# Kernel optimization log

Hardware: AMD Instinct MI355X
Metric: run time of the kernel (lower is better)

## Reference

```python
import jax, jax.numpy as jnp
import numpy as np
import math

C = 512
B, T = 8, 2048
STRIDE = 2
LN_EPS = 1e-5
EPS = 1e-8


def _ln(x, g, b):
    mu = jnp.mean(x, axis=-1, keepdims=True)
    var = jnp.mean(jnp.square(x - mu), axis=-1, keepdims=True)
    return (x - mu) * jax.lax.rsqrt(var + LN_EPS) * g + b


def _lin(x, w, b):
    # torch Linear: y = x @ W^T + b, W: [out, in]
    return jnp.einsum('btc,oc->bto', x, w) + b


def setup_inputs() -> dict:
    key = jax.random.key(0)
    ks = iter(jax.random.split(key, 40))
    s = 0.02
    d = {'x': jax.random.normal(next(ks), (B, T, C), jnp.float32)}
    # downsample conv: [C_out, C_in, K]
    d['dw'] = jax.random.normal(next(ks), (C, C, 3), jnp.float32) * s
    d['db'] = jnp.zeros((C,), jnp.float32)
    for br in ('cr', 'd', 'c'):
        for p in ('q', 'k', 'v'):
            d[f'w{p}_{br}'] = jax.random.normal(next(ks), (C, C), jnp.float32) * s
            d[f'b{p}_{br}'] = jnp.zeros((C,), jnp.float32)
        d[f'ln_{br}_g'] = jnp.ones((C,), jnp.float32)
        d[f'ln_{br}_b'] = jnp.zeros((C,), jnp.float32)
    d['temp'] = jnp.asarray(0.1, jnp.float32)
    d['gw'] = jax.random.normal(next(ks), (3, 3 * C), jnp.float32) * s  # conv1d k=1 squeezed
    d['gb'] = jnp.zeros((3,), jnp.float32)
    return d


def _forward(x, dw, db, wq_cr, bq_cr, wk_cr, bk_cr, wv_cr, bv_cr, ln_cr_g, ln_cr_b,
             wq_d, bq_d, wk_d, bk_d, wv_d, bv_d, ln_d_g, ln_d_b,
             wq_c, bq_c, wk_c, bk_c, wv_c, bv_c, ln_c_g, ln_c_b,
             temp, gw, gb):
    scale = 1.0 / math.sqrt(C)
    # downsample: Conv1d(k=3, stride, pad=1) on [B,C,T]
    xc = jnp.transpose(x, (0, 2, 1))
    xd = jax.lax.conv_general_dilated(
        xc, dw, window_strides=(STRIDE,), padding=[(1, 1)],
        dimension_numbers=('NCH', 'OIH', 'NCH')) + db[None, :, None]
    x_down = jnp.transpose(xd, (0, 2, 1))  # [B, T//2, C]

    # cross-resolution branch
    q = _lin(x, wq_cr, bq_cr)
    k = _lin(x_down, wk_cr, bk_cr)
    v = _lin(x_down, wv_cr, bv_cr)
    a = jax.nn.softmax(jnp.einsum('btc,bsc->bts', q, k) * scale, axis=-1)
    out_cross = _ln(jnp.einsum('bts,bsc->btc', a, v), ln_cr_g, ln_cr_b)

    # dot-product branch
    q = _lin(x, wq_d, bq_d)
    k = _lin(x, wk_d, bk_d)
    v = _lin(x, wv_d, bv_d)
    a = jax.nn.softmax(jnp.einsum('btc,bsc->bts', q, k) * scale, axis=-1)
    out_dot = _ln(jnp.einsum('bts,bsc->btc', a, v), ln_d_g, ln_d_b)

    # cosine branch with learnable temperature
    q = _lin(x, wq_c, bq_c)
    k = _lin(x, wk_c, bk_c)
    qn = q / (jnp.linalg.norm(q, axis=2, keepdims=True) + EPS)
    kn = k / (jnp.linalg.norm(k, axis=2, keepdims=True) + EPS)
    t = jnp.maximum(temp, 0.01)
    a = jax.nn.softmax(jnp.einsum('btc,bsc->bts', qn, kn) / t, axis=-1)
    v = _lin(x, wv_c, bv_c)
    out_cos = _ln(jnp.einsum('bts,bsc->btc', a, v), ln_c_g, ln_c_b)

    # learned gating fusion (conv1d k=1 == per-position linear over 3C)
    fused = jnp.concatenate([out_cross, out_dot, out_cos], axis=-1)  # [B,T,3C]
    gate = jax.nn.softmax(jnp.einsum('btc,gc->btg', fused, gw) + gb, axis=-1)  # [B,T,3]
    z = (gate[..., 0:1] * out_cross + gate[..., 1:2] * out_dot + gate[..., 2:3] * out_cos)
    return z


def reference(x, dw, db, wq_cr, bq_cr, wk_cr, bk_cr, wv_cr, bv_cr, ln_cr_g, ln_cr_b,
              wq_d, bq_d, wk_d, bk_d, wv_d, bv_d, ln_d_g, ln_d_b,
              wq_c, bq_c, wk_c, bk_c, wv_c, bv_c, ln_c_g, ln_c_b,
              temp, gw, gb):
    return _forward(x, dw, db, wq_cr, bq_cr, wk_cr, bk_cr, wv_cr, bv_cr, ln_cr_g, ln_cr_b,
                    wq_d, bq_d, wk_d, bk_d, wv_d, bv_d, ln_d_g, ln_d_b,
                    wq_c, bq_c, wk_c, bk_c, wv_c, bv_c, ln_c_g, ln_c_b,
                    temp, gw, gb)
```

## Files before the change

kernel.cpp:

```cpp
#include <hip/hip_runtime.h>


typedef __attribute__((ext_vector_type(8))) __bf16 bf16x8;
typedef __attribute__((ext_vector_type(4))) float f32x4;

#define CDIM 512
#define TFULL 2048

#define GLL16(gp, lp)                                                        \
  __builtin_amdgcn_global_load_lds(                                          \
      (const __attribute__((address_space(1))) unsigned int*)(gp),           \
      (__attribute__((address_space(3))) unsigned int*)(lp), 16, 0, 0)

__device__ __forceinline__ unsigned short f2bf(float f) {
  unsigned u = __float_as_uint(f);
  u = (u + 0x7fffu + ((u >> 16) & 1u)) >> 16;
  return (unsigned short)u;
}
__device__ __forceinline__ float bf2f(unsigned short h) {
  return __uint_as_float(((unsigned)h) << 16);
}

__global__ __launch_bounds__(256)
void k_tobf16(const float* __restrict__ src, unsigned short* __restrict__ dst, long n4) {
  long i = (long)blockIdx.x * 256 + threadIdx.x;
  if (i >= n4) return;
  float4 f = reinterpret_cast<const float4*>(src)[i];
  unsigned short o4[4] = {f2bf(f.x), f2bf(f.y), f2bf(f.z), f2bf(f.w)};
  reinterpret_cast<uint2*>(dst)[i] = *reinterpret_cast<const uint2*>(o4);
}

struct WPtrs { const float* p[9]; };
__global__ __launch_bounds__(256)
void k_tobf16w(WPtrs w, unsigned short* __restrict__ dst) {
  int idx = blockIdx.x * 256 + threadIdx.x;
  if (idx >= 9 * 65536) return;
  int m = idx >> 16, off = idx & 65535;
  float4 f = reinterpret_cast<const float4*>(w.p[m])[off];
  unsigned short o4[4] = {f2bf(f.x), f2bf(f.y), f2bf(f.z), f2bf(f.w)};
  reinterpret_cast<uint2*>(dst + (long)m * 262144)[off] = *reinterpret_cast<const uint2*>(o4);
}

__global__ __launch_bounds__(256)
void k_dwreorder(const float* __restrict__ dw, unsigned short* __restrict__ dwb) {
  int idx = blockIdx.x * 256 + threadIdx.x;
  if (idx >= 512 * 1536) return;
  int o = idx / 1536, rem = idx - o * 1536;
  int k = rem >> 9, i = rem & 511;
  dwb[idx] = f2bf(dw[(o * 512 + i) * 3 + k]);
}

__global__ __launch_bounds__(256)
void k_im2col(const float* __restrict__ x, unsigned short* __restrict__ aim) {
  long idx = (long)blockIdx.x * 256 + threadIdx.x;
  if (idx >= (long)8192 * 1536 / 4) return;
  long e = idx * 4;
  int row = (int)(e / 1536);
  int col = (int)(e - (long)row * 1536);
  int b = row >> 10, t = row & 1023;
  int k = col >> 9, i = col & 511;
  int r = 2 * t - 1 + k;
  float4 f = {0.f, 0.f, 0.f, 0.f};
  if (r >= 0) f = *reinterpret_cast<const float4*>(x + ((long)b * TFULL + r) * CDIM + i);
  unsigned short o4[4] = {f2bf(f.x), f2bf(f.y), f2bf(f.z), f2bf(f.w)};
  *reinterpret_cast<uint2*>(aim + e) = *reinterpret_cast<const uint2*>(o4);
}

__global__ __launch_bounds__(256)
void k_gemm(const unsigned short* __restrict__ A,
            const unsigned short* __restrict__ B,
            void* __restrict__ Cp,
            int K, int lda, int ldb, int ldc,
            long sA, long sB, long sC,
            const float* __restrict__ bias,
            float alpha, const float* __restrict__ tempPtr,
            int mode, int ldct) {
  const int gx = gridDim.x;
  const int nwg = gx * gridDim.y;
  int wg = blockIdx.x + gx * blockIdx.y;
  wg = (wg & 7) * (nwg >> 3) + (wg >> 3);
  const int tm0 = (wg % gx) * 128, tn0 = (wg / gx) * 128;
  const int bz = blockIdx.z;
  const unsigned short* Ag = A + (long)bz * sA;
  const unsigned short* Bg = B + (long)bz * sB;

  __shared__ __align__(16) unsigned short smem[32768];

  const int tid = threadIdx.x;
  const int lane = tid & 63;
  const int wave = tid >> 6;
  const int wm = (wave >> 1) * 64, wn = (wave & 1) * 64;
  const int lrow = lane & 15, kq = lane >> 4;

  f32x4 acc[4][4];
#pragma unroll
  for (int i = 0; i < 4; ++i)
#pragma unroll
    for (int j = 0; j < 4; ++j) acc[i][j] = f32x4{0.f, 0.f, 0.f, 0.f};

  const int sr = tid >> 3;
  const int sj = (tid & 7) ^ (sr & 7);
  const unsigned short* aSrc = Ag + (long)(tm0 + sr) * lda + sj * 8;
  const unsigned short* bSrc = Bg + (long)(tn0 + sr) * ldb + sj * 8;

  const int nt = K >> 6;

#define STAGE(kt_, buf_)                                                     \
  {                                                                          \
    unsigned short* aD = smem + (buf_) * 8192 + wave * 512;                  \
    unsigned short* bD = smem + 16384 + (buf_) * 8192 + wave * 512;          \
    _Pragma("unroll")                                                        \
    for (int rd = 0; rd < 4; ++rd) {                                         \
      GLL16(aSrc + (kt_) + (long)rd * 32 * lda, aD + rd * 2048);             \
      GLL16(bSrc + (kt_) + (long)rd * 32 * ldb, bD + rd * 2048);             \
    }                                                                        \
  }

  STAGE(0, 0);

  const int xr = (lrow & 7) << 3;
  for (int t = 0; t < nt; ++t) {
    __syncthreads();
    if (t + 1 < nt) STAGE((t + 1) << 6, (t + 1) & 1);
    const unsigned short* As_ = smem + (t & 1) * 8192;
    const unsigned short* Bs_ = smem + 16384 + (t & 1) * 8192;
    bf16x8 af[4][2], bfv[4][2];
#pragma unroll
    for (int mi = 0; mi < 4; ++mi)
#pragma unroll
      for (int ks = 0; ks < 2; ++ks)
        af[mi][ks] = *reinterpret_cast<const bf16x8*>(
            &As_[(wm + mi * 16 + lrow) * 64 + ((ks * 32 + kq * 8) ^ xr)]);
#pragma unroll
    for (int ni = 0; ni < 4; ++ni)
#pragma unroll
      for (int ks = 0; ks < 2; ++ks)
        bfv[ni][ks] = *reinterpret_cast<const bf16x8*>(
            &Bs_[(wn + ni * 16 + lrow) * 64 + ((ks * 32 + kq * 8) ^ xr)]);
#pragma unroll
    for (int mi = 0; mi < 4; ++mi)
#pragma unroll
      for (int ni = 0; ni < 4; ++ni) {
        acc[mi][ni] = __builtin_amdgcn_mfma_f32_16x16x32_bf16(af[mi][0], bfv[ni][0], acc[mi][ni], 0, 0, 0);
        acc[mi][ni] = __builtin_amdgcn_mfma_f32_16x16x32_bf16(af[mi][1], bfv[ni][1], acc[mi][ni], 0, 0, 0);
      }
  }
#undef STAGE

  if (tempPtr) alpha = 1.0f / fmaxf(*tempPtr, 0.01f);

  if (mode == 1) {
    unsigned short* Cb = (unsigned short*)Cp + (long)bz * sC;
#pragma unroll
    for (int mi = 0; mi < 4; ++mi) {
      int rg = tm0 + wm + mi * 16 + kq * 4;
#pragma unroll
      for (int ni = 0; ni < 4; ++ni) {
        int cg = tn0 + wn + ni * 16 + lrow;
        float bb = bias ? bias[cg] : 0.f;
        f32x4 v = acc[mi][ni];
#pragma unroll
        for (int r = 0; r < 4; ++r)
          Cb[(long)(rg + r) * ldc + cg] = f2bf(v[r] * alpha + bb);
      }
    }
  } else {
    unsigned short* Cb = (unsigned short*)Cp + (long)bz * sC;
#pragma unroll
    for (int mi = 0; mi < 4; ++mi) {
      int rg = tm0 + wm + mi * 16 + kq * 4;
#pragma unroll
      for (int ni = 0; ni < 4; ++ni) {
        int cg = tn0 + wn + ni * 16 + lrow;
        float bb = bias ? bias[cg] : 0.f;
        f32x4 v = acc[mi][ni];
#pragma unroll
        for (int r = 0; r < 4; ++r)
          Cb[(long)cg * ldct + (rg + r)] = f2bf(v[r] * alpha + bb);
      }
    }
  }
}

__global__ __launch_bounds__(512)
void k_gemm256(const unsigned short* __restrict__ A,
               const unsigned short* __restrict__ B,
               unsigned short* __restrict__ C,
               int K, int lda, int ldb, int ldc,
               long sA, long sB, long sC,
               float alpha, const float* __restrict__ tempPtr) {
  const int gx = gridDim.x;
  const int nwg = gx * gridDim.y;
  int wg = blockIdx.x + gx * blockIdx.y;
  wg = (wg & 7) * (nwg >> 3) + (wg >> 3);
  const int tm0 = (wg % gx) * 256, tn0 = (wg / gx) * 256;
  const unsigned short* Ag = A + (long)blockIdx.z * sA;
  const unsigned short* Bg = B + (long)blockIdx.z * sB;

  __shared__ __align__(16) unsigned short smem[32768];

  const int tid = threadIdx.x;
  const int lane = tid & 63;
  const int wave = tid >> 6;
  const int wm = (wave >> 2) * 128, wn = (wave & 3) * 64;
  const int lrow = lane & 15, kq = lane >> 4;

  f32x4 acc[8][4];
#pragma unroll
  for (int i = 0; i < 8; ++i)
#pragma unroll
    for (int j = 0; j < 4; ++j) acc[i][j] = f32x4{0.f, 0.f, 0.f, 0.f};

  const int srow = lane >> 2;
  const int sslot = (lane & 3) ^ ((lane >> 3) & 3);
  const unsigned short* aS0 = Ag + (long)(tm0 + wave * 16 + srow) * lda + sslot * 8;
  const unsigned short* aS1 = aS0 + 128L * lda;
  const unsigned short* bS0 = Bg + (long)(tn0 + wave * 16 + srow) * ldb + sslot * 8;
  const unsigned short* bS1 = bS0 + 128L * ldb;

  const int nt = K >> 5;

#define STAGE256(kt_, buf_)                                                  \
  {                                                                          \
    unsigned short* aD = smem + (buf_) * 8192 + wave * 512;                  \
    unsigned short* bD = smem + 16384 + (buf_) * 8192 + wave * 512;          \
    GLL16(aS0 + (kt_), aD);                                                  \
    GLL16(aS1 + (kt_), aD + 4096);                                           \
    GLL16(bS0 + (kt_), bD);                                                  \
    GLL16(bS1 + (kt_), bD + 4096);                                           \
  }

  STAGE256(0, 0);

  const int xr = ((lrow >> 1) & 3) << 3;
  for (int t = 0; t < nt; ++t) {
    if (t + 1 < nt) {
      STAGE256((t + 1) << 5, (t + 1) & 1);
      asm volatile("s_waitcnt vmcnt(4)" ::: "memory");
    } else {
      asm volatile("s_waitcnt vmcnt(0)" ::: "memory");
    }
    __builtin_amdgcn_s_barrier();
    __builtin_amdgcn_sched_barrier(0);
    const unsigned short* As_ = smem + (t & 1) * 8192;
    const unsigned short* Bs_ = smem + 16384 + (t & 1) * 8192;
    bf16x8 bfv[4];
#pragma unroll
    for (int ni = 0; ni < 4; ++ni)
      bfv[ni] = *reinterpret_cast<const bf16x8*>(
          &Bs_[(wn + ni * 16 + lrow) * 32 + ((kq * 8) ^ xr)]);
#pragma unroll
    for (int mi = 0; mi < 8; ++mi) {
      bf16x8 af = *reinterpret_cast<const bf16x8*>(
          &As_[(wm + mi * 16 + lrow) * 32 + ((kq * 8) ^ xr)]);
#pragma unroll
      for (int ni = 0; ni < 4; ++ni)
        acc[mi][ni] = __builtin_amdgcn_mfma_f32_16x16x32_bf16(af, bfv[ni], acc[mi][ni], 0, 0, 0);
    }
    __builtin_amdgcn_sched_barrier(0);
    if (t + 1 < nt) __builtin_amdgcn_s_barrier();
  }
#undef STAGE256

  if (tempPtr) alpha = 1.0f / fmaxf(*tempPtr, 0.01f);

  C += (long)blockIdx.z * sC;
#pragma unroll
  for (int mi = 0; mi < 8; ++mi) {
    int rg = tm0 + wm + mi * 16 + kq * 4;
#pragma unroll
    for (int ni = 0; ni < 4; ++ni) {
      int cg = tn0 + wn + ni * 16 + lrow;
      f32x4 v = acc[mi][ni];
#pragma unroll
      for (int r = 0; r < 4; ++r)
        C[(long)(rg + r) * ldc + cg] = f2bf(v[r] * alpha);
    }
  }
}

__global__ __launch_bounds__(256)
void k_softmax(unsigned short* __restrict__ S, int cols) {
  const long base = (long)blockIdx.x * cols;
  const int tid = threadIdx.x, lane = tid & 63, wave = tid >> 6;
  const int nv = cols >> 3;
  float f[8];
  float mx = -3.0e38f;
  if (tid < nv) {
    uint4 v = *reinterpret_cast<const uint4*>(S + base + tid * 8);
    const unsigned short* pv = (const unsigned short*)&v;
#pragma unroll
    for (int j = 0; j < 8; ++j) { f[j] = bf2f(pv[j]); mx = fmaxf(mx, f[j]); }
  }
  __shared__ float rmax[4], rsum[4];
#pragma unroll
  for (int o = 32; o > 0; o >>= 1) mx = fmaxf(mx, __shfl_down(mx, o));
  if (lane == 0) rmax[wave] = mx;
  __syncthreads();
  mx = fmaxf(fmaxf(rmax[0], rmax[1]), fmaxf(rmax[2], rmax[3]));
  float sum = 0.f;
  if (tid < nv) {
#pragma unroll
    for (int j = 0; j < 8; ++j) { f[j] = __expf(f[j] - mx); sum += f[j]; }
  }
#pragma unroll
  for (int o = 32; o > 0; o >>= 1) sum += __shfl_down(sum, o);
  if (lane == 0) rsum[wave] = sum;
  __syncthreads();
  const float inv = 1.0f / (rsum[0] + rsum[1] + rsum[2] + rsum[3]);
  if (tid < nv) {
    unsigned short o8[8];
#pragma unroll
    for (int j = 0; j < 8; ++j) o8[j] = f2bf(f[j] * inv);
    *reinterpret_cast<uint4*>(S + base + tid * 8) = *reinterpret_cast<const uint4*>(o8);
  }
}

__global__ __launch_bounds__(256)
void k_l2norm(unsigned short* __restrict__ Q, int ld) {
  const int lane = threadIdx.x & 63, wave = threadIdx.x >> 6;
  const long row = (long)blockIdx.x * 4 + wave;
  unsigned short* p = Q + row * ld + lane * 8;
  uint4 v = *reinterpret_cast<const uint4*>(p);
  const unsigned short* pv = (const unsigned short*)&v;
  float f[8]; float q = 0.f;
#pragma unroll
  for (int j = 0; j < 8; ++j) { f[j] = bf2f(pv[j]); q += f[j] * f[j]; }
#pragma unroll
  for (int o = 32; o > 0; o >>= 1) q += __shfl_xor(q, o);
  float sc = 1.0f / (sqrtf(q) + 1e-8f);
  unsigned short o8[8];
#pragma unroll
  for (int j = 0; j < 8; ++j) o8[j] = f2bf(f[j] * sc);
  *reinterpret_cast<uint4*>(p) = *reinterpret_cast<const uint4*>(o8);
}

__global__ __launch_bounds__(256)
void k_ln_bf(unsigned short* __restrict__ X, const float* __restrict__ g,
             const float* __restrict__ b) {
  const int lane = threadIdx.x & 63, wave = threadIdx.x >> 6;
  const long row = (long)blockIdx.x * 4 + wave;
  unsigned short* p = X + row * CDIM + lane * 8;
  uint4 v = *reinterpret_cast<const uint4*>(p);
  const unsigned short* pv = (const unsigned short*)&v;
  float f[8];
  float s = 0.f, q = 0.f;
#pragma unroll
  for (int j = 0; j < 8; ++j) { f[j] = bf2f(pv[j]); s += f[j]; q += f[j] * f[j]; }
#pragma unroll
  for (int o = 32; o > 0; o >>= 1) { s += __shfl_xor(s, o); q += __shfl_xor(q, o); }
  float mu = s * (1.f / 512.f);
  float var = q * (1.f / 512.f) - mu * mu;
  float rs = rsqrtf(var + 1e-5f);
  float gg[8], bb[8];
  *reinterpret_cast<float4*>(&gg[0]) = *reinterpret_cast<const float4*>(g + lane * 8);
  *reinterpret_cast<float4*>(&gg[4]) = *reinterpret_cast<const float4*>(g + lane * 8 + 4);
  *reinterpret_cast<float4*>(&bb[0]) = *reinterpret_cast<const float4*>(b + lane * 8);
  *reinterpret_cast<float4*>(&bb[4]) = *reinterpret_cast<const float4*>(b + lane * 8 + 4);
  unsigned short o8[8];
#pragma unroll
  for (int j = 0; j < 8; ++j) o8[j] = f2bf((f[j] - mu) * rs * gg[j] + bb[j]);
  *reinterpret_cast<uint4*>(p) = *reinterpret_cast<const uint4*>(o8);
}

__global__ __launch_bounds__(256)
void k_gate(const unsigned short* __restrict__ o0, const unsigned short* __restrict__ o1,
            const unsigned short* __restrict__ o2, const float* __restrict__ gw,
            const float* __restrict__ gb, float* __restrict__ out) {
  __shared__ float gws[3 * 1536];
  for (int i = threadIdx.x; i < 3 * 1536; i += 256) gws[i] = gw[i];
  __syncthreads();
  const int lane = threadIdx.x & 63, wave = threadIdx.x >> 6;
  const long pos = (long)blockIdx.x * 4 + wave;
  const long off = pos * CDIM + lane * 8;
  float a[8], bq[8], cq[8];
  {
    uint4 va = *reinterpret_cast<const uint4*>(o0 + off);
    uint4 vb = *reinterpret_cast<const uint4*>(o1 + off);
    uint4 vc = *reinterpret_cast<const uint4*>(o2 + off);
    const unsigned short* pa = (const unsigned short*)&va;
    const unsigned short* pb = (const unsigned short*)&vb;
    const unsigned short* pc = (const unsigned short*)&vc;
#pragma unroll
    for (int j = 0; j < 8; ++j) { a[j] = bf2f(pa[j]); bq[j] = bf2f(pb[j]); cq[j] = bf2f(pc[j]); }
  }
  float l0 = 0.f, l1 = 0.f, l2 = 0.f;
  const int ch = lane * 8;
#pragma unroll
  for (int j = 0; j < 8; ++j) {
    l0 += a[j] * gws[ch + j] + bq[j] * gws[512 + ch + j] + cq[j] * gws[1024 + ch + j];
    l1 += a[j] * gws[1536 + ch + j] + bq[j] * gws[2048 + ch + j] + cq[j] * gws[2560 + ch + j];
    l2 += a[j] * gws[3072 + ch + j] + bq[j] * gws[3584 + ch + j] + cq[j] * gws[4096 + ch + j];
  }
#pragma unroll
  for (int o = 32; o > 0; o >>= 1) {
    l0 += __shfl_xor(l0, o); l1 += __shfl_xor(l1, o); l2 += __shfl_xor(l2, o);
  }
  l0 += gb[0]; l1 += gb[1]; l2 += gb[2];
  float m = fmaxf(l0, fmaxf(l1, l2));
  float e0 = __expf(l0 - m), e1 = __expf(l1 - m), e2 = __expf(l2 - m);
  float inv = 1.f / (e0 + e1 + e2);
  float g0 = e0 * inv, g1 = e1 * inv, g2 = e2 * inv;
  float r[8];
#pragma unroll
  for (int j = 0; j < 8; ++j) r[j] = g0 * a[j] + g1 * bq[j] + g2 * cq[j];
  *reinterpret_cast<float4*>(out + off) = *reinterpret_cast<const float4*>(&r[0]);
  *reinterpret_cast<float4*>(out + off + 4) = *reinterpret_cast<const float4*>(&r[4]);
}

extern "C" void kernel_launch(void* const* d_in, const int* in_sizes, int n_in,
                              void* d_out, int out_size, void* d_ws, size_t ws_size,
                              hipStream_t stream) {
  (void)in_sizes; (void)n_in; (void)out_size;
  const float* x = (const float*)d_in[0];
  const float* dw = (const float*)d_in[1];
  const float* db = (const float*)d_in[2];
  WPtrs wp;
  wp.p[0] = (const float*)d_in[3];  wp.p[1] = (const float*)d_in[5];
  wp.p[2] = (const float*)d_in[7];  wp.p[3] = (const float*)d_in[11];
  wp.p[4] = (const float*)d_in[13]; wp.p[5] = (const float*)d_in[15];
  wp.p[6] = (const float*)d_in[19]; wp.p[7] = (const float*)d_in[21];
  wp.p[8] = (const float*)d_in[23];
  const float* bq_cr = (const float*)d_in[4];
  const float* bk_cr = (const float*)d_in[6];
  const float* bv_cr = (const float*)d_in[8];
  const float* ln_cr_g = (const float*)d_in[9];
  const float* ln_cr_b = (const float*)d_in[10];
  const float* bq_d = (const float*)d_in[12];
  const float* bk_d = (const float*)d_in[14];
  const float* bv_d = (const float*)d_in[16];
  const float* ln_d_g = (const float*)d_in[17];
  const float* ln_d_b = (const float*)d_in[18];
  const float* bq_c = (const float*)d_in[20];
  const float* bk_c = (const float*)d_in[22];
  const float* bv_c = (const float*)d_in[24];
  const float* ln_c_g = (const float*)d_in[25];
  const float* ln_c_b = (const float*)d_in[26];
  const float* temp = (const float*)d_in[27];
  const float* gw = (const float*)d_in[28];
  const float* gb = (const float*)d_in[29];

  if (ws_size < 240000000ULL) return;

  char* p = (char*)d_ws;
  auto alloc = [&](size_t bytes) {
    void* r = (void*)p;
    p += (bytes + 255) & ~(size_t)255;
    return r;
  };
  unsigned short* XB  = (unsigned short*)alloc(16384L * 512 * 2);
  unsigned short* XD  = (unsigned short*)alloc(8192L * 512 * 2);
  unsigned short* WB  = (unsigned short*)alloc(9L * 262144 * 2);
  unsigned short* DWB = (unsigned short*)alloc(512L * 1536 * 2);
  unsigned short* QB  = (unsigned short*)alloc(16384L * 512 * 2);
  unsigned short* KB  = (unsigned short*)alloc(8192L * 512 * 2);
  unsigned short* VTB = (unsigned short*)alloc(16384L * 512 * 2);
  unsigned short* OUT0 = (unsigned short*)alloc(16384L * 512 * 2);
  unsigned short* OUT1 = (unsigned short*)alloc(16384L * 512 * 2);
  unsigned short* OUT2 = (unsigned short*)alloc(16384L * 512 * 2);
  unsigned short* QK2 = (unsigned short*)alloc(16384L * 1024 * 2);
  float* BC = (float*)alloc(2048 * 4);
  unsigned short* SB = (unsigned short*)alloc(8L * 2048 * 2048 * 2);
  unsigned short* AIM = SB;

  const float scale = 0.044194173824159216f;

  auto gemm = [&](const unsigned short* A, const unsigned short* Bm, void* Cm,
                  int M, int N, int K, int lda, int ldb, int ldc,
                  int batch, long sA, long sB, long sC,
                  const float* bias, float alpha, const float* tp, int mode, int ldct) {
    dim3 g(M / 128, N / 128, batch);
    k_gemm<<<g, 256, 0, stream>>>(A, Bm, Cm, K, lda, ldb, ldc, sA, sB, sC,
                                  bias, alpha, tp, mode, ldct);
  };
  auto gemm256 = [&](const unsigned short* A, const unsigned short* Bm,
                     unsigned short* Cm, int M, int N, int K,
                     int lda, int ldb, int ldc, int batch,
                     long sA, long sB, long sC, float alpha, const float* tp) {
    dim3 g(M / 256, N / 256, batch);
    k_gemm256<<<g, 512, 0, stream>>>(A, Bm, Cm, K, lda, ldb, ldc, sA, sB, sC, alpha, tp);
  };

  k_tobf16<<<8192, 256, 0, stream>>>(x, XB, 16384L * 512 / 4);
  k_tobf16w<<<2304, 256, 0, stream>>>(wp, WB);
  k_dwreorder<<<3072, 256, 0, stream>>>(dw, DWB);
  k_im2col<<<12288, 256, 0, stream>>>(x, AIM);
  hipMemcpyAsync(BC,        bq_d, 512 * 4, hipMemcpyDeviceToDevice, stream);
  hipMemcpyAsync(BC + 512,  bk_d, 512 * 4, hipMemcpyDeviceToDevice, stream);
  hipMemcpyAsync(BC + 1024, bq_c, 512 * 4, hipMemcpyDeviceToDevice, stream);
  hipMemcpyAsync(BC + 1536, bk_c, 512 * 4, hipMemcpyDeviceToDevice, stream);

  gemm(AIM, DWB, XD, 8192, 512, 1536, 1536, 1536, 512, 1, 0, 0, 0,
       db, 1.f, nullptr, 1, 0);

  gemm(XB, WB + 0 * 262144L, QB, 16384, 512, 512, 512, 512, 512, 1, 0, 0, 0,
       bq_cr, 1.f, nullptr, 1, 0);
  gemm(XD, WB + 1 * 262144L, KB, 8192, 512, 512, 512, 512, 512, 1, 0, 0, 0,
       bk_cr, 1.f, nullptr, 1, 0);
  gemm(XD, WB + 2 * 262144L, VTB, 1024, 512, 512, 512, 512, 0, 8,
       1024L * 512, 0, 512L * 1024, bv_cr, 1.f, nullptr, 2, 1024);
  gemm256(QB, KB, SB, 2048, 1024, 512, 512, 512, 1024, 8,
          2048L * 512, 1024L * 512, 2048L * 1024, scale, nullptr);
  k_softmax<<<16384, 256, 0, stream>>>(SB, 1024);
  gemm(SB, VTB, OUT0, 2048, 512, 1024, 1024, 1024, 512, 8,
       2048L * 1024, 512L * 1024, 2048L * 512, nullptr, 1.f, nullptr, 1, 0);
  k_ln_bf<<<4096, 256, 0, stream>>>(OUT0, ln_cr_g, ln_cr_b);

  gemm(XB, WB + 3 * 262144L, QK2, 16384, 1024, 512, 512, 512, 1024, 1, 0, 0, 0,
       BC, 1.f, nullptr, 1, 0);
  gemm(XB, WB + 5 * 262144L, VTB, 2048, 512, 512, 512, 512, 0, 8,
       2048L * 512, 0, 512L * 2048, bv_d, 1.f, nullptr, 2, 2048);
  gemm256(QK2, QK2 + 512, SB, 2048, 2048, 512, 1024, 1024, 2048, 8,
          2048L * 1024, 2048L * 1024, 2048L * 2048, scale, nullptr);
  k_softmax<<<16384, 256, 0, stream>>>(SB, 2048);
  gemm(SB, VTB, OUT1, 2048, 512, 2048, 2048, 2048, 512, 8,
       2048L * 2048, 512L * 2048, 2048L * 512, nullptr, 1.f, nullptr, 1, 0);
  k_ln_bf<<<4096, 256, 0, stream>>>(OUT1, ln_d_g, ln_d_b);

  gemm(XB, WB + 6 * 262144L, QK2, 16384, 1024, 512, 512, 512, 1024, 1, 0, 0, 0,
       BC + 1024, 1.f, nullptr, 1, 0);
  k_l2norm<<<4096, 256, 0, stream>>>(QK2, 1024);
  k_l2norm<<<4096, 256, 0, stream>>>(QK2 + 512, 1024);
  gemm(XB, WB + 8 * 262144L, VTB, 2048, 512, 512, 512, 512, 0, 8,
       2048L * 512, 0, 512L * 2048, bv_c, 1.f, nullptr, 2, 2048);
  gemm256(QK2, QK2 + 512, SB, 2048, 2048, 512, 1024, 1024, 2048, 8,
          2048L * 1024, 2048L * 1024, 2048L * 2048, 1.f, temp);
  k_softmax<<<16384, 256, 0, stream>>>(SB, 2048);
  gemm(SB, VTB, OUT2, 2048, 512, 2048, 2048, 2048, 512, 8,
       2048L * 2048, 512L * 2048, 2048L * 512, nullptr, 1.f, nullptr, 1, 0);
  k_ln_bf<<<4096, 256, 0, stream>>>(OUT2, ln_c_g, ln_c_b);

  k_gate<<<4096, 256, 0, stream>>>(OUT0, OUT1, OUT2, gw, gb, (float*)d_out);
}
```

Baseline: 567.2 us.

## Drop im2col via strided-view conv GEMM, pipeline k_gemm barriers, use 256-tile QK projections

The separate im2col kernel is removed. The stride-2 conv now reads the bf16 input directly as an overlapping view, with a row stride of 1024 starting 512 elements before each batch. A small fix-up kernel recomputes output row 0, where that view would otherwise pick up the padding region. The 128-tile GEMM main loop now issues the next stage's loads before waiting on the current one, using explicit vmcnt waits and split barriers, to overlap loads with MFMA work. The fused Q/K projections switch to the 256-tile GEMM, which gains bias support, and the weight order is permuted to make room for the pair layout. The extra alloc(1024) guard keeps the XB-512 read in bounds, but the row-0 fix-up adds a serial dot-product kernel.

```diff
diff --git a/kernel.cpp b/kernel.cpp
--- a/kernel.cpp
+++ b/kernel.cpp
@@ -51,19 +51,16 @@
 }
 
 __global__ __launch_bounds__(256)
-void k_im2col(const float* __restrict__ x, unsigned short* __restrict__ aim) {
-  long idx = (long)blockIdx.x * 256 + threadIdx.x;
-  if (idx >= (long)8192 * 1536 / 4) return;
-  long e = idx * 4;
-  int row = (int)(e / 1536);
-  int col = (int)(e - (long)row * 1536);
-  int b = row >> 10, t = row & 1023;
-  int k = col >> 9, i = col & 511;
-  int r = 2 * t - 1 + k;
-  float4 f = {0.f, 0.f, 0.f, 0.f};
-  if (r >= 0) f = *reinterpret_cast<const float4*>(x + ((long)b * TFULL + r) * CDIM + i);
-  unsigned short o4[4] = {f2bf(f.x), f2bf(f.y), f2bf(f.z), f2bf(f.w)};
-  *reinterpret_cast<uint2*>(aim + e) = *reinterpret_cast<const uint2*>(o4);
+void k_fix(const unsigned short* __restrict__ XB, const unsigned short* __restrict__ DWB,
+           const float* __restrict__ db, unsigned short* __restrict__ XD) {
+  int idx = blockIdx.x * 256 + threadIdx.x;
+  if (idx >= 4096) return;
+  int b = idx >> 9, o = idx & 511;
+  const unsigned short* xr = XB + (long)b * TFULL * CDIM;
+  const unsigned short* wr = DWB + (long)o * 1536 + 512;
+  float acc = db[o];
+  for (int i = 0; i < 1024; ++i) acc += bf2f(xr[i]) * bf2f(wr[i]);
+  XD[(long)b * 1024 * 512 + o] = f2bf(acc);
 }
 
 __global__ __launch_bounds__(256)
@@ -120,8 +117,14 @@
 
   const int xr = (lrow & 7) << 3;
   for (int t = 0; t < nt; ++t) {
-    __syncthreads();
-    if (t + 1 < nt) STAGE((t + 1) << 6, (t + 1) & 1);
+    if (t + 1 < nt) {
+      STAGE((t + 1) << 6, (t + 1) & 1);
+      asm volatile("s_waitcnt vmcnt(8)" ::: "memory");
+    } else {
+      asm volatile("s_waitcnt vmcnt(0)" ::: "memory");
+    }
+    __builtin_amdgcn_s_barrier();
+    __builtin_amdgcn_sched_barrier(0);
     const unsigned short* As_ = smem + (t & 1) * 8192;
     const unsigned short* Bs_ = smem + 16384 + (t & 1) * 8192;
     bf16x8 af[4][2], bfv[4][2];
@@ -144,6 +147,8 @@
         acc[mi][ni] = __builtin_amdgcn_mfma_f32_16x16x32_bf16(af[mi][0], bfv[ni][0], acc[mi][ni], 0, 0, 0);
         acc[mi][ni] = __builtin_amdgcn_mfma_f32_16x16x32_bf16(af[mi][1], bfv[ni][1], acc[mi][ni], 0, 0, 0);
       }
+    __builtin_amdgcn_sched_barrier(0);
+    if (t + 1 < nt) __builtin_amdgcn_s_barrier();
   }
 #undef STAGE
 
@@ -188,6 +193,7 @@
                unsigned short* __restrict__ C,
                int K, int lda, int ldb, int ldc,
                long sA, long sB, long sC,
+               const float* __restrict__ bias,
                float alpha, const float* __restrict__ tempPtr) {
   const int gx = gridDim.x;
   const int nwg = gx * gridDim.y;
@@ -271,10 +277,11 @@
 #pragma unroll
     for (int ni = 0; ni < 4; ++ni) {
       int cg = tn0 + wn + ni * 16 + lrow;
+      float bb = bias ? bias[cg] : 0.f;
       f32x4 v = acc[mi][ni];
 #pragma unroll
       for (int r = 0; r < 4; ++r)
-        C[(long)(rg + r) * ldc + cg] = f2bf(v[r] * alpha);
+        C[(long)(rg + r) * ldc + cg] = f2bf(v[r] * alpha + bb);
     }
   }
 }
@@ -416,11 +423,15 @@
   const float* dw = (const float*)d_in[1];
   const float* db = (const float*)d_in[2];
   WPtrs wp;
-  wp.p[0] = (const float*)d_in[3];  wp.p[1] = (const float*)d_in[5];
-  wp.p[2] = (const float*)d_in[7];  wp.p[3] = (const float*)d_in[11];
-  wp.p[4] = (const float*)d_in[13]; wp.p[5] = (const float*)d_in[15];
-  wp.p[6] = (const float*)d_in[19]; wp.p[7] = (const float*)d_in[21];
-  wp.p[8] = (const float*)d_in[23];
+  wp.p[0] = (const float*)d_in[3];
+  wp.p[1] = (const float*)d_in[11];
+  wp.p[2] = (const float*)d_in[13];
+  wp.p[3] = (const float*)d_in[19];
+  wp.p[4] = (const float*)d_in[21];
+  wp.p[5] = (const float*)d_in[15];
+  wp.p[6] = (const float*)d_in[23];
+  wp.p[7] = (const float*)d_in[5];
+  wp.p[8] = (const float*)d_in[7];
   const float* bq_cr = (const float*)d_in[4];
   const float* bk_cr = (const float*)d_in[6];
   const float* bv_cr = (const float*)d_in[8];
@@ -448,20 +459,20 @@
     p += (bytes + 255) & ~(size_t)255;
     return r;
   };
+  alloc(1024);
   unsigned short* XB  = (unsigned short*)alloc(16384L * 512 * 2);
   unsigned short* XD  = (unsigned short*)alloc(8192L * 512 * 2);
   unsigned short* WB  = (unsigned short*)alloc(9L * 262144 * 2);
   unsigned short* DWB = (unsigned short*)alloc(512L * 1536 * 2);
   unsigned short* QB  = (unsigned short*)alloc(16384L * 512 * 2);
   unsigned short* KB  = (unsigned short*)alloc(8192L * 512 * 2);
-  unsigned short* VTB = (unsigned short*)alloc(16384L * 512 * 2);
+  unsigned short* VT  = (unsigned short*)alloc(512L * 16384 * 2);
   unsigned short* OUT0 = (unsigned short*)alloc(16384L * 512 * 2);
   unsigned short* OUT1 = (unsigned short*)alloc(16384L * 512 * 2);
   unsigned short* OUT2 = (unsigned short*)alloc(16384L * 512 * 2);
   unsigned short* QK2 = (unsigned short*)alloc(16384L * 1024 * 2);
   float* BC = (float*)alloc(2048 * 4);
   unsigned short* SB = (unsigned short*)alloc(8L * 2048 * 2048 * 2);
-  unsigned short* AIM = SB;
 
   const float scale = 0.044194173824159216f;
 
@@ -476,57 +487,59 @@
   auto gemm256 = [&](const unsigned short* A, const unsigned short* Bm,
                      unsigned short* Cm, int M, int N, int K,
                      int lda, int ldb, int ldc, int batch,
-                     long sA, long sB, long sC, float alpha, const float* tp) {
+                     long sA, long sB, long sC,
+                     const float* bias, float alpha, const float* tp) {
     dim3 g(M / 256, N / 256, batch);
-    k_gemm256<<<g, 512, 0, stream>>>(A, Bm, Cm, K, lda, ldb, ldc, sA, sB, sC, alpha, tp);
+    k_gemm256<<<g, 512, 0, stream>>>(A, Bm, Cm, K, lda, ldb, ldc, sA, sB, sC,
+                                     bias, alpha, tp);
   };
 
   k_tobf16<<<8192, 256, 0, stream>>>(x, XB, 16384L * 512 / 4);
   k_tobf16w<<<2304, 256, 0, stream>>>(wp, WB);
   k_dwreorder<<<3072, 256, 0, stream>>>(dw, DWB);
-  k_im2col<<<12288, 256, 0, stream>>>(x, AIM);
   hipMemcpyAsync(BC,        bq_d, 512 * 4, hipMemcpyDeviceToDevice, stream);
   hipMemcpyAsync(BC + 512,  bk_d, 512 * 4, hipMemcpyDeviceToDevice, stream);
   hipMemcpyAsync(BC + 1024, bq_c, 512 * 4, hipMemcpyDeviceToDevice, stream);
   hipMemcpyAsync(BC + 1536, bk_c, 512 * 4, hipMemcpyDeviceToDevice, stream);
 
-  gemm(AIM, DWB, XD, 8192, 512, 1536, 1536, 1536, 512, 1, 0, 0, 0,
-       db, 1.f, nullptr, 1, 0);
+  gemm(XB - 512, DWB, XD, 1024, 512, 1536, 1024, 1536, 512,
+       8, 1048576L, 0, 524288L, db, 1.f, nullptr, 1, 0);
+  k_fix<<<16, 256, 0, stream>>>(XB, DWB, db, XD);
 
   gemm(XB, WB + 0 * 262144L, QB, 16384, 512, 512, 512, 512, 512, 1, 0, 0, 0,
        bq_cr, 1.f, nullptr, 1, 0);
-  gemm(XD, WB + 1 * 262144L, KB, 8192, 512, 512, 512, 512, 512, 1, 0, 0, 0,
+  gemm(XD, WB + 7 * 262144L, KB, 8192, 512, 512, 512, 512, 512, 1, 0, 0, 0,
        bk_cr, 1.f, nullptr, 1, 0);
-  gemm(XD, WB + 2 * 262144L, VTB, 1024, 512, 512, 512, 512, 0, 8,
+  gemm(XD, WB + 8 * 262144L, VT, 1024, 512, 512, 512, 512, 0, 8,
        1024L * 512, 0, 512L * 1024, bv_cr, 1.f, nullptr, 2, 1024);
   gemm256(QB, KB, SB, 2048, 1024, 512, 512, 512, 1024, 8,
-          2048L * 512, 1024L * 512, 2048L * 1024, scale, nullptr);
+          2048L * 512, 1024L * 512, 2048L * 1024, nullptr, scale, nullptr);
   k_softmax<<<16384, 256, 0, stream>>>(SB, 1024);
-  gemm(SB, VTB, OUT0, 2048, 512, 1024, 1024, 1024, 512, 8,
+  gemm(SB, VT, OUT0, 2048, 512, 1024, 1024, 1024, 512, 8,
        2048L * 1024, 512L * 1024, 2048L * 512, nullptr, 1.f, nullptr, 1, 0);
   k_ln_bf<<<4096, 256, 0, stream>>>(OUT0, ln_cr_g, ln_cr_b);
 
-  gemm(XB, WB + 3 * 262144L, QK2, 16384, 1024, 512, 512, 512, 1024, 1, 0, 0, 0,
-       BC, 1.f, nullptr, 1, 0);
-  gemm(XB, WB + 5 * 262144L, VTB, 2048, 512, 512, 512, 512, 0, 8,
+  gemm256(XB, WB + 1 * 262144L, QK2, 16384, 1024, 512, 512, 512, 1024,
+          1, 0, 0, 0, BC, 1.f, nullptr);
+  gemm(XB, WB + 5 * 262144L, VT, 2048, 512, 512, 512, 512, 0, 8,
        2048L * 512, 0, 512L * 2048, bv_d, 1.f, nullptr, 2, 2048);
   gemm256(QK2, QK2 + 512, SB, 2048, 2048, 512, 1024, 1024, 2048, 8,
-          2048L * 1024, 2048L * 1024, 2048L * 2048, scale, nullptr);
+          2048L * 1024, 2048L * 1024, 2048L * 2048, nullptr, scale, nullptr);
   k_softmax<<<16384, 256, 0, stream>>>(SB, 2048);
-  gemm(SB, VTB, OUT1, 2048, 512, 2048, 2048, 2048, 512, 8,
+  gemm(SB, VT, OUT1, 2048, 512, 2048, 2048, 2048, 512, 8,
        2048L * 2048, 512L * 2048, 2048L * 512, nullptr, 1.f, nullptr, 1, 0);
   k_ln_bf<<<4096, 256, 0, stream>>>(OUT1, ln_d_g, ln_d_b);
 
-  gemm(XB, WB + 6 * 262144L, QK2, 16384, 1024, 512, 512, 512, 1024, 1, 0, 0, 0,
-       BC + 1024, 1.f, nullptr, 1, 0);
+  gemm256(XB, WB + 3 * 262144L, QK2, 16384, 1024, 512, 512, 512, 1024,
+          1, 0, 0, 0, BC + 1024, 1.f, nullptr);
   k_l2norm<<<4096, 256, 0, stream>>>(QK2, 1024);
   k_l2norm<<<4096, 256, 0, stream>>>(QK2 + 512, 1024);
-  gemm(XB, WB + 8 * 262144L, VTB, 2048, 512, 512, 512, 512, 0, 8,
+  gemm(XB, WB + 6 * 262144L, VT, 2048, 512, 512, 512, 512, 0, 8,
        2048L * 512, 0, 512L * 2048, bv_c, 1.f, nullptr, 2, 2048);
   gemm256(QK2, QK2 + 512, SB, 2048, 2048, 512, 1024, 1024, 2048, 8,
-          2048L * 1024, 2048L * 1024, 2048L * 2048, 1.f, temp);
+          2048L * 1024, 2048L * 1024, 2048L * 2048, nullptr, 1.f, temp);
   k_softmax<<<16384, 256, 0, stream>>>(SB, 2048);
-  gemm(SB, VTB, OUT2, 2048, 512, 2048, 2048, 2048, 512, 8,
+  gemm(SB, VT, OUT2, 2048, 512, 2048, 2048, 2048, 512, 8,
        2048L * 2048, 512L * 2048, 2048L * 512, nullptr, 1.f, nullptr, 1, 0);
   k_ln_bf<<<4096, 256, 0, stream>>>(OUT2, ln_c_g, ln_c_b);
 
```

New measurement: 584.6 us. 1.03x slower.
